# Kernel optimization log

Measured on AMD Instinct MI355X. Metric: run time of the kernel, lower is better.

Reference implementation:

```python
import jax, jax.numpy as jnp
import numpy as np

N_USERS = 100000
N_ITEMS = 50000
N = N_USERS + N_ITEMS  # graph nodes
E = 2_400_000
B = 16384
EMB = 64
HID = 128
LN_EPS = 1e-5


def _gcn(x, W, b, src, dst):
    # PyG GCNConv (eval): sym-normalized aggregation with self-loops.
    xw = x @ W                                      # [N, out]
    deg = jnp.ones((N,), x.dtype).at[dst].add(1.0)  # in-degree + self-loop
    dinv = jax.lax.rsqrt(deg)
    norm = dinv[src] * dinv[dst]                    # [E]
    msg = xw[src] * norm[:, None]                   # [E, out] gather
    out = jax.ops.segment_sum(msg, dst, num_segments=N)
    out = out + xw * (dinv * dinv)[:, None]         # self-loop term (norm_ii = 1/deg_i)
    return out + b


def _ln(h, g, b):
    mu = jnp.mean(h, axis=-1, keepdims=True)
    var = jnp.mean(jnp.square(h - mu), axis=-1, keepdims=True)
    return (h - mu) * jax.lax.rsqrt(var + LN_EPS) * g + b


def setup_inputs() -> dict:
    key = jax.random.key(0)
    ks = jax.random.split(key, 20)
    f32 = jnp.float32
    def lin(k, fi, fo):
        return jax.random.normal(k, (fi, fo), f32) * (1.0 / np.sqrt(fi))
    inp = {
        "x": jax.random.normal(ks[0], (N, EMB), f32),
        "src": jax.random.randint(ks[1], (E,), 0, N, jnp.int32),
        "dst": jax.random.randint(ks[2], (E,), 0, N, jnp.int32),
        "user_indices": jax.random.randint(ks[3], (B,), 1, N_USERS + 1, jnp.int32),
        "item_indices": jax.random.randint(ks[4], (B,), 1, N_ITEMS + 1, jnp.int32),
        # GCNConv weights
        "W1": lin(ks[5], EMB, HID), "b1": jnp.zeros((HID,), f32),
        "W2": lin(ks[6], HID, EMB), "b2": jnp.zeros((EMB,), f32),
        # MLP head: Linear(128,128)-LN-ReLU-Linear(128,64)-LN-ReLU-Linear(64,1)
        "fcW1": lin(ks[7], 2 * EMB, HID), "fcb1": jnp.zeros((HID,), f32),
        "g1": jnp.ones((HID,), f32), "be1": jnp.zeros((HID,), f32),
        "fcW2": lin(ks[8], HID, HID // 2), "fcb2": jnp.zeros((HID // 2,), f32),
        "g2": jnp.ones((HID // 2,), f32), "be2": jnp.zeros((HID // 2,), f32),
        "fcW3": lin(ks[9], HID // 2, 1), "fcb3": jnp.zeros((1,), f32),
    }
    return inp


def reference(x, src, dst, user_indices, item_indices,
              W1, b1, W2, b2,
              fcW1, fcb1, g1, be1, fcW2, fcb2, g2, be2, fcW3, fcb3):
    # graph path (edge_index and x provided); dropout inactive in eval mode
    h = jax.nn.relu(_gcn(x, W1, b1, src, dst))
    h = _gcn(h, W2, b2, src, dst)                   # [N, EMB]
    user_emb = h[:N_USERS][user_indices - 1]        # [B, EMB]
    item_emb = h[N_USERS:][item_indices - 1]        # [B, EMB]
    c = jnp.concatenate([user_emb, item_emb], axis=1)  # [B, 2*EMB]
    z = jax.nn.relu(_ln(c @ fcW1 + fcb1, g1, be1))
    z = jax.nn.relu(_ln(z @ fcW2 + fcb2, g2, be2))
    z = z @ fcW3 + fcb3                             # [B, 1]
    return jax.nn.sigmoid(z).squeeze()
```

## Files before the change

kernel.cpp:

```cpp
#include <hip/hip_runtime.h>
#include <hip/hip_bf16.h>
#include <math.h>

#define N_USERS_C 100000
#define BK_SHIFT 9
#define BK_NODES 512
#define CPAD 16

typedef __bf16 bf8_t __attribute__((ext_vector_type(8)));
typedef float f32x4 __attribute__((ext_vector_type(4)));

__device__ __forceinline__ unsigned int pack_bf16(float a, float b) {
    __hip_bfloat16 ha = __float2bfloat16(a), hb = __float2bfloat16(b);
    return ((unsigned int)(*(unsigned short*)&hb) << 16) | (unsigned int)(*(unsigned short*)&ha);
}
__device__ __forceinline__ unsigned short bf16_1(float a) {
    __hip_bfloat16 ha = __float2bfloat16(a);
    return *(unsigned short*)&ha;
}
__device__ __forceinline__ float bf_lo(unsigned int u) { return __uint_as_float(u << 16); }
__device__ __forceinline__ float bf_hi(unsigned int u) { return __uint_as_float(u & 0xffff0000u); }

__global__ __launch_bounds__(512) void k_pre(const int* __restrict__ dst, int* __restrict__ chist,
                                             const float* __restrict__ x, unsigned int* __restrict__ xb,
                                             const float* __restrict__ W1, const float* __restrict__ W2,
                                             unsigned int* __restrict__ w1p, unsigned int* __restrict__ w2p,
                                             int E, int nbk, int EB2, int n2, int XB) {
    __shared__ int lcnt[BK_NODES];
    const int bid = blockIdx.x;
    const int t = threadIdx.x;
    if (bid < EB2) {
        if (t < nbk) lcnt[t] = 0;
        __syncthreads();
        int e0 = bid * 4096;
        #pragma unroll
        for (int j = 0; j < 8; ++j) {
            int e = e0 + j * 512 + t;
            if (e < E) atomicAdd(&lcnt[dst[e] >> BK_SHIFT], 1);
        }
        __syncthreads();
        if (t < nbk && lcnt[t]) atomicAdd(&chist[t * CPAD], lcnt[t]);
    } else if (bid < EB2 + XB) {
        int base = (bid - EB2) * 2048;
        #pragma unroll
        for (int j = 0; j < 4; ++j) {
            int i = base + j * 512 + t;
            if (i < n2) {
                float2 v = ((const float2*)x)[i];
                xb[i] = pack_bf16(v.x, v.y);
            }
        }
    } else if (bid == EB2 + XB) {
        #pragma unroll
        for (int j = 0; j < 8; ++j) {
            int i = j * 512 + t;
            int kp = i >> 7, n = i & 127;
            w1p[n * 32 + kp] = pack_bf16(W1[(size_t)(2 * kp) * 128 + n],
                                         W1[(size_t)(2 * kp + 1) * 128 + n]);
        }
    } else {
        #pragma unroll
        for (int j = 0; j < 8; ++j) {
            int i = j * 512 + t;
            int kp = i >> 6, n = i & 63;
            w2p[n * 64 + kp] = pack_bf16(W2[(size_t)(2 * kp) * 64 + n],
                                         W2[(size_t)(2 * kp + 1) * 64 + n]);
        }
    }
}

__global__ __launch_bounds__(512) void k_bin(const int* __restrict__ src,
                                             const int* __restrict__ dst,
                                             const int* __restrict__ chist,
                                             int* __restrict__ bcursor0,
                                             int* __restrict__ pairBuf, int E, int nbk) {
    __shared__ int lcnt[BK_NODES];
    __shared__ int lofs[BK_NODES];
    __shared__ int delta[BK_NODES];
    __shared__ int waveSum[8];
    __shared__ int sPack[4096];
    __shared__ unsigned short sBkt[4096];
    const int t = threadIdx.x;
    const int lane = t & 63;
    const int w = t >> 6;
    const int e0 = blockIdx.x * 4096;
    if (t < nbk) lcnt[t] = 0;
    __syncthreads();

    int mySrc[8], myB[8], myDl[8];
    #pragma unroll
    for (int j = 0; j < 8; ++j) {
        int e = e0 + j * 512 + t;
        if (e < E) {
            int sv = src[e], dv = dst[e];
            mySrc[j] = sv; myB[j] = dv >> BK_SHIFT; myDl[j] = dv & (BK_NODES - 1);
            atomicAdd(&lcnt[myB[j]], 1);
        } else myB[j] = -1;
    }
    __syncthreads();

    int v = (t < nbk) ? lcnt[t] : 0;
    int inc = v;
    #pragma unroll
    for (int off = 1; off < 64; off <<= 1) {
        int n = __shfl_up(inc, off);
        if (lane >= off) inc += n;
    }
    if (lane == 63) waveSum[w] = inc;
    int cv = (t < nbk) ? chist[t * CPAD] : 0;
    int cinc = cv;
    #pragma unroll
    for (int off = 1; off < 64; off <<= 1) {
        int n = __shfl_up(cinc, off);
        if (lane >= off) cinc += n;
    }
    __shared__ int cWaveSum[8];
    if (lane == 63) cWaveSum[w] = cinc;
    __syncthreads();
    int wp = 0, cwp = 0;
    #pragma unroll
    for (int i = 0; i < 8; ++i) {
        wp += (i < w) ? waveSum[i] : 0;
        cwp += (i < w) ? cWaveSum[i] : 0;
    }
    int ex = wp + inc - v;
    int cbase = cwp + cinc - cv;
    if (t < nbk) {
        lofs[t] = ex;
        int gb = cbase + ((v > 0) ? atomicAdd(&bcursor0[t * CPAD], v) : 0);
        delta[t] = gb - ex;
    }
    __syncthreads();

    #pragma unroll
    for (int j = 0; j < 8; ++j) {
        if (myB[j] >= 0) {
            int p = atomicAdd(&lofs[myB[j]], 1);
            sPack[p] = mySrc[j] | (myDl[j] << 18);
            sBkt[p] = (unsigned short)myB[j];
        }
    }
    __syncthreads();
    int total = (E - e0 < 4096) ? (E - e0) : 4096;
    for (int i = t; i < total; i += 512)
        pairBuf[delta[sBkt[i]] + i] = sPack[i];
}

__global__ __launch_bounds__(512) void k_bscatter(const int* __restrict__ pairBuf,
                                                  const int* __restrict__ chist,
                                                  int* __restrict__ rowstart,
                                                  float* __restrict__ dinv,
                                                  int* __restrict__ csr,
                                                  unsigned int* __restrict__ xb,
                                                  int N, int E, int nbk) {
    const int b = blockIdx.x;
    const int n0 = b << BK_SHIFT;
    int nn = N - n0; if (nn > BK_NODES) nn = BK_NODES;
    __shared__ int hist[BK_NODES];
    __shared__ int curs[BK_NODES];
    __shared__ float sdv[BK_NODES];
    __shared__ int waveSum[8];
    __shared__ int sE0, sE1;
    const int t = threadIdx.x;
    const int lane = t & 63;
    const int w = t >> 6;

    {
        int cv = (t < nbk) ? chist[t * CPAD] : 0;
        int cinc = cv;
        #pragma unroll
        for (int off = 1; off < 64; off <<= 1) {
            int n = __shfl_up(cinc, off);
            if (lane >= off) cinc += n;
        }
        if (lane == 63) waveSum[w] = cinc;
        if (t < nn) hist[t] = 0;
        __syncthreads();
        int cwp = 0;
        #pragma unroll
        for (int i = 0; i < 8; ++i) cwp += (i < w) ? waveSum[i] : 0;
        if (t == b) { sE0 = cwp + cinc - cv; sE1 = cwp + cinc; }
    }
    __syncthreads();
    const int e0 = sE0, e1 = sE1;

    for (int e = e0 + t; e < e1; e += 512)
        atomicAdd(&hist[pairBuf[e] >> 18], 1);
    __syncthreads();

    int v = (t < nn) ? hist[t] : 0;
    int inc = v;
    #pragma unroll
    for (int off = 1; off < 64; off <<= 1) {
        int n = __shfl_up(inc, off);
        if (lane >= off) inc += n;
    }
    if (lane == 63) waveSum[w] = inc;
    __syncthreads();
    int wp = 0;
    #pragma unroll
    for (int i = 0; i < 8; ++i) wp += (i < w) ? waveSum[i] : 0;
    int ex = wp + inc - v;
    if (t < nn) {
        int r = e0 + ex;
        rowstart[n0 + t] = r;
        curs[t] = r;
        float dv = rsqrtf((float)(v + 1));
        dinv[n0 + t] = dv;
        sdv[t] = dv;
    }
    if (b == gridDim.x - 1 && t == 0) rowstart[N] = E;
    __syncthreads();
    for (int e = e0 + t; e < e1; e += 512) {
        int pk = pairBuf[e];
        int pos = atomicAdd(&curs[pk >> 18], 1);
        csr[pos] = pk & 0x3FFFF;
    }
    {
        uint4* xb4 = (uint4*)(xb + (size_t)n0 * 32);
        int tot = nn * 8;
        for (int j = t; j < tot; j += 512) {
            float dv = sdv[j >> 3];
            uint4 u = xb4[j];
            u.x = pack_bf16(dv * bf_lo(u.x), dv * bf_hi(u.x));
            u.y = pack_bf16(dv * bf_lo(u.y), dv * bf_hi(u.y));
            u.z = pack_bf16(dv * bf_lo(u.z), dv * bf_hi(u.z));
            u.w = pack_bf16(dv * bf_lo(u.w), dv * bf_hi(u.w));
            xb4[j] = u;
        }
    }
}

__global__ __launch_bounds__(256) void k_gather1(const int* __restrict__ rowstart,
                                                 const int* __restrict__ csr,
                                                 const float* __restrict__ dinv,
                                                 const uint4* __restrict__ xb4,
                                                 unsigned int* __restrict__ outb, int N) {
    const int node = blockIdx.x * 4 + (threadIdx.x >> 6);
    const int l = threadIdx.x & 63;
    if (node >= N) return;
    const int sub = l >> 3;
    const int c = l & 7;
    const int rs = rowstart[node];
    const int re = rowstart[node + 1];
    uint4 us = xb4[(size_t)node * 8 + c];
    float dd = dinv[node];

    float acc[8] = {0.f, 0.f, 0.f, 0.f, 0.f, 0.f, 0.f, 0.f};
    for (int base = rs; base < re; base += 64) {
        int idx = base + l;
        int sE = (idx < re) ? csr[idx] : 0;
        int cnt = re - base; if (cnt > 64) cnt = 64;
        int groups = (cnt + 7) >> 3;
        int sk = __shfl(sE, sub);
        uint4 u = xb4[(size_t)sk * 8 + c];
        for (int g = 0; g < groups; ++g) {
            uint4 ucur = u;
            if (g + 1 < groups) {
                int skn = __shfl(sE, (g + 1) * 8 + sub);
                u = xb4[(size_t)skn * 8 + c];
            }
            if (g * 8 + sub < cnt) {
                acc[0] += bf_lo(ucur.x); acc[1] += bf_hi(ucur.x);
                acc[2] += bf_lo(ucur.y); acc[3] += bf_hi(ucur.y);
                acc[4] += bf_lo(ucur.z); acc[5] += bf_hi(ucur.z);
                acc[6] += bf_lo(ucur.w); acc[7] += bf_hi(ucur.w);
            }
        }
    }
    #pragma unroll
    for (int m = 8; m < 64; m <<= 1)
        #pragma unroll
        for (int i = 0; i < 8; ++i) acc[i] += __shfl_xor(acc[i], m);
    if (sub == 0) {
        uint4 o;
        o.x = pack_bf16(dd * (acc[0] + bf_lo(us.x)), dd * (acc[1] + bf_hi(us.x)));
        o.y = pack_bf16(dd * (acc[2] + bf_lo(us.y)), dd * (acc[3] + bf_hi(us.y)));
        o.z = pack_bf16(dd * (acc[4] + bf_lo(us.z)), dd * (acc[5] + bf_hi(us.z)));
        o.w = pack_bf16(dd * (acc[6] + bf_lo(us.w)), dd * (acc[7] + bf_hi(us.w)));
        ((uint4*)outb)[(size_t)node * 8 + c] = o;
    }
}

__global__ __launch_bounds__(256) void k_layer12(const unsigned int* __restrict__ aggXb,
                                                 const unsigned int* __restrict__ w1p,
                                                 const float* __restrict__ b1,
                                                 const unsigned int* __restrict__ w2p,
                                                 const float* __restrict__ dinv,
                                                 unsigned int* __restrict__ xs2b, int N) {
    __shared__ unsigned int sA[64 * 36];
    __shared__ unsigned int sB[128 * 36];
    __shared__ unsigned int sC[64 * 68];
    const int t = threadIdx.x;
    const int w = t >> 6;
    const int l = t & 63;
    const int n16 = l & 15;
    const int quad = l >> 4;
    const int row0 = blockIdx.x * 64;

    for (int i = t; i < 512; i += 256) {
        int r = i >> 3, c = i & 7;
        int row = row0 + r;
        uint4 u = (row < N) ? ((const uint4*)aggXb)[(size_t)row * 8 + c]
                            : make_uint4(0u, 0u, 0u, 0u);
        *(uint4*)&sA[r * 36 + c * 4] = u;
    }
    {
        const uint4* w1p4 = (const uint4*)w1p;
        for (int j = t; j < 1024; j += 256) {
            int n = j >> 3, kp4 = j & 7;
            *(uint4*)&sB[n * 36 + kp4 * 4] = w1p4[j];
        }
    }
    __syncthreads();

    f32x4 acc[8];
    #pragma unroll
    for (int nt = 0; nt < 8; ++nt) acc[nt] = (f32x4){0.f, 0.f, 0.f, 0.f};
    {
        const int am = w * 16 + n16;
        bf8_t a0 = *(const bf8_t*)&sA[am * 36 + quad * 4];
        bf8_t a1 = *(const bf8_t*)&sA[am * 36 + 16 + quad * 4];
        #pragma unroll
        for (int nt = 0; nt < 8; ++nt) {
            bf8_t b0 = *(const bf8_t*)&sB[(nt * 16 + n16) * 36 + quad * 4];
            bf8_t b1v = *(const bf8_t*)&sB[(nt * 16 + n16) * 36 + 16 + quad * 4];
            acc[nt] = __builtin_amdgcn_mfma_f32_16x16x32_bf16(a0, b0, acc[nt], 0, 0, 0);
            acc[nt] = __builtin_amdgcn_mfma_f32_16x16x32_bf16(a1, b1v, acc[nt], 0, 0, 0);
        }
    }
    __syncthreads();

    {
        unsigned short* sC16 = (unsigned short*)sC;
        #pragma unroll
        for (int nt = 0; nt < 8; ++nt) {
            int col = nt * 16 + n16;
            float bv = b1[col];
            #pragma unroll
            for (int reg = 0; reg < 4; ++reg) {
                int r = w * 16 + quad * 4 + reg;
                sC16[r * 136 + col] = bf16_1(fmaxf(acc[nt][reg] + bv, 0.f));
            }
        }
    }
    {
        const uint4* w2p4 = (const uint4*)w2p;
        for (int j = t; j < 1024; j += 256) {
            int n = j >> 4, kp4 = j & 15;
            *(uint4*)&sB[n * 68 + kp4 * 4] = w2p4[j];
        }
    }
    __syncthreads();

    f32x4 acc2[4];
    #pragma unroll
    for (int nt = 0; nt < 4; ++nt) acc2[nt] = (f32x4){0.f, 0.f, 0.f, 0.f};
    {
        const int am = w * 16 + n16;
        #pragma unroll
        for (int ks = 0; ks < 4; ++ks) {
            bf8_t a = *(const bf8_t*)&sC[am * 68 + ks * 16 + quad * 4];
            #pragma unroll
            for (int nt = 0; nt < 4; ++nt) {
                bf8_t b = *(const bf8_t*)&sB[(nt * 16 + n16) * 68 + ks * 16 + quad * 4];
                acc2[nt] = __builtin_amdgcn_mfma_f32_16x16x32_bf16(a, b, acc2[nt], 0, 0, 0);
            }
        }
    }

    __syncthreads();
    {
        unsigned short* sA16 = (unsigned short*)sA;
        #pragma unroll
        for (int reg = 0; reg < 4; ++reg) {
            int r = w * 16 + quad * 4 + reg;
            int row = row0 + r;
            float dd = (row < N) ? dinv[row] : 0.f;
            #pragma unroll
            for (int nt = 0; nt < 4; ++nt)
                sA16[r * 72 + nt * 16 + n16] = bf16_1(acc2[nt][reg] * dd);
        }
    }
    __syncthreads();
    for (int i = t; i < 512; i += 256) {
        int r = i >> 3, c = i & 7;
        int row = row0 + r;
        if (row < N)
            ((uint4*)xs2b)[(size_t)row * 8 + c] = *(uint4*)&sA[r * 36 + c * 4];
    }
}

__global__ __launch_bounds__(256) void k_gather_pairs(const int* __restrict__ rowstart,
                                                      const int* __restrict__ csr,
                                                      const float* __restrict__ dinv,
                                                      const uint4* __restrict__ xs2b4,
                                                      const float* __restrict__ b2,
                                                      const int* __restrict__ ui,
                                                      const int* __restrict__ ii,
                                                      float* __restrict__ cB, int B) {
    const int wave = threadIdx.x >> 6;
    const int b = blockIdx.x * 2 + (wave >> 1);
    const int half = wave & 1;
    const int l = threadIdx.x & 63;
    const int sub = l >> 3;
    const int c = l & 7;
    if (b >= B) return;
    const int node = (half == 0) ? (ui[b] - 1) : (N_USERS_C + ii[b] - 1);
    const int rs = rowstart[node];
    const int re = rowstart[node + 1];
    uint4 us = xs2b4[(size_t)node * 8 + c];
    float dd = dinv[node];

    float acc[8] = {0.f, 0.f, 0.f, 0.f, 0.f, 0.f, 0.f, 0.f};
    for (int base = rs; base < re; base += 64) {
        int idx = base + l;
        int sE = (idx < re) ? csr[idx] : 0;
        int cnt = re - base; if (cnt > 64) cnt = 64;
        int groups = (cnt + 7) >> 3;
        int sk = __shfl(sE, sub);
        uint4 u = xs2b4[(size_t)sk * 8 + c];
        for (int g = 0; g < groups; ++g) {
            uint4 ucur = u;
            if (g + 1 < groups) {
                int skn = __shfl(sE, (g + 1) * 8 + sub);
                u = xs2b4[(size_t)skn * 8 + c];
            }
            if (g * 8 + sub < cnt) {
                acc[0] += bf_lo(ucur.x); acc[1] += bf_hi(ucur.x);
                acc[2] += bf_lo(ucur.y); acc[3] += bf_hi(ucur.y);
                acc[4] += bf_lo(ucur.z); acc[5] += bf_hi(ucur.z);
                acc[6] += bf_lo(ucur.w); acc[7] += bf_hi(ucur.w);
            }
        }
    }
    #pragma unroll
    for (int m = 8; m < 64; m <<= 1)
        #pragma unroll
        for (int i = 0; i < 8; ++i) acc[i] += __shfl_xor(acc[i], m);
    if (sub == 0) {
        float4 s0, s1;
        s0.x = bf_lo(us.x); s0.y = bf_hi(us.x); s0.z = bf_lo(us.y); s0.w = bf_hi(us.y);
        s1.x = bf_lo(us.z); s1.y = bf_hi(us.z); s1.z = bf_lo(us.w); s1.w = bf_hi(us.w);
        float4 bb0 = ((const float4*)b2)[c * 2];
        float4 bb1 = ((const float4*)b2)[c * 2 + 1];
        float4 o0, o1;
        o0.x = dd * (acc[0] + s0.x) + bb0.x;
        o0.y = dd * (acc[1] + s0.y) + bb0.y;
        o0.z = dd * (acc[2] + s0.z) + bb0.z;
        o0.w = dd * (acc[3] + s0.w) + bb0.w;
        o1.x = dd * (acc[4] + s1.x) + bb1.x;
        o1.y = dd * (acc[5] + s1.y) + bb1.y;
        o1.z = dd * (acc[6] + s1.z) + bb1.z;
        o1.w = dd * (acc[7] + s1.w) + bb1.w;
        ((float4*)cB)[(size_t)b * 32 + half * 16 + c * 2] = o0;
        ((float4*)cB)[(size_t)b * 32 + half * 16 + c * 2 + 1] = o1;
    }
}

__global__ __launch_bounds__(256) void k_mlp(const float* __restrict__ cB,
                                             const float* __restrict__ fcW1, const float* __restrict__ fcb1,
                                             const float* __restrict__ g1,   const float* __restrict__ be1,
                                             const float* __restrict__ fcW2, const float* __restrict__ fcb2,
                                             const float* __restrict__ g2,   const float* __restrict__ be2,
                                             const float* __restrict__ fcW3, const float* __restrict__ fcb3,
                                             float* __restrict__ out) {
    __shared__ float sIn[32 * 128];
    __shared__ float sW[64 * 128];
    const int t = threadIdx.x;
    const int row0 = blockIdx.x * 32;
    const int rg = t >> 4;
    const int cg = t & 15;

    for (int i = t; i < 1024; i += 256) {
        int r = i >> 5, c4 = i & 31;
        *(float4*)&sIn[r * 128 + c4 * 4] = *(const float4*)&cB[(size_t)(row0 + r) * 128 + c4 * 4];
    }

    float acc1[2][8];
    {
        float4 b01 = *(const float4*)&fcb1[cg * 8];
        float4 b23 = *(const float4*)&fcb1[cg * 8 + 4];
        #pragma unroll
        for (int jj = 0; jj < 2; ++jj) {
            acc1[jj][0] = b01.x; acc1[jj][1] = b01.y; acc1[jj][2] = b01.z; acc1[jj][3] = b01.w;
            acc1[jj][4] = b23.x; acc1[jj][5] = b23.y; acc1[jj][6] = b23.z; acc1[jj][7] = b23.w;
        }
    }
    for (int s = 0; s < 2; ++s) {
        __syncthreads();
        for (int i = t; i < 2048; i += 256) {
            int k = i >> 5, c4 = i & 31;
            *(float4*)&sW[k * 128 + c4 * 4] = *(const float4*)&fcW1[(size_t)(64 * s + k) * 128 + c4 * 4];
        }
        __syncthreads();
        for (int k0 = 0; k0 < 64; k0 += 4) {
            float4 a[2];
            #pragma unroll
            for (int jj = 0; jj < 2; ++jj)
                a[jj] = *(const float4*)&sIn[(rg * 2 + jj) * 128 + 64 * s + k0];
            #pragma unroll
            for (int kk = 0; kk < 4; ++kk) {
                float4 w0 = *(const float4*)&sW[(k0 + kk) * 128 + cg * 8];
                float4 w1 = *(const float4*)&sW[(k0 + kk) * 128 + cg * 8 + 4];
                #pragma unroll
                for (int jj = 0; jj < 2; ++jj) {
                    float f = ((const float*)&a[jj])[kk];
                    acc1[jj][0] += f * w0.x; acc1[jj][1] += f * w0.y;
                    acc1[jj][2] += f * w0.z; acc1[jj][3] += f * w0.w;
                    acc1[jj][4] += f * w1.x; acc1[jj][5] += f * w1.y;
                    acc1[jj][6] += f * w1.z; acc1[jj][7] += f * w1.w;
                }
            }
        }
    }
    __syncthreads();

    {
        float4 g01 = *(const float4*)&g1[cg * 8];
        float4 g23 = *(const float4*)&g1[cg * 8 + 4];
        float4 e01 = *(const float4*)&be1[cg * 8];
        float4 e23 = *(const float4*)&be1[cg * 8 + 4];
        float gv[8] = {g01.x, g01.y, g01.z, g01.w, g23.x, g23.y, g23.z, g23.w};
        float ev[8] = {e01.x, e01.y, e01.z, e01.w, e23.x, e23.y, e23.z, e23.w};
        #pragma unroll
        for (int jj = 0; jj < 2; ++jj) {
            float s_ = 0.f, ss = 0.f;
            #pragma unroll
            for (int c = 0; c < 8; ++c) { float v = acc1[jj][c]; s_ += v; ss += v * v; }
            #pragma unroll
            for (int m = 1; m < 16; m <<= 1) { s_ += __shfl_xor(s_, m); ss += __shfl_xor(ss, m); }
            float mu = s_ * (1.0f / 128.0f);
            float var = ss * (1.0f / 128.0f) - mu * mu;
            float rs = rsqrtf(var + 1e-5f);
            #pragma unroll
            for (int c = 0; c < 8; ++c) {
                float z = (acc1[jj][c] - mu) * rs * gv[c] + ev[c];
                sIn[(rg * 2 + jj) * 128 + cg * 8 + c] = fmaxf(z, 0.f);
            }
        }
    }
    __syncthreads();

    for (int i = t; i < 2048; i += 256) {
        int k = i >> 4, c4 = i & 15;
        *(float4*)&sW[k * 64 + c4 * 4] = *(const float4*)&fcW2[(size_t)k * 64 + c4 * 4];
    }
    float acc2[2][4];
    {
        float4 bv = *(const float4*)&fcb2[cg * 4];
        #pragma unroll
        for (int jj = 0; jj < 2; ++jj) {
            acc2[jj][0] = bv.x; acc2[jj][1] = bv.y; acc2[jj][2] = bv.z; acc2[jj][3] = bv.w;
        }
    }
    __syncthreads();
    for (int k0 = 0; k0 < 128; k0 += 4) {
        float4 a[2], w[4];
        #pragma unroll
        for (int jj = 0; jj < 2; ++jj) a[jj] = *(const float4*)&sIn[(rg * 2 + jj) * 128 + k0];
        #pragma unroll
        for (int kk = 0; kk < 4; ++kk) w[kk] = *(const float4*)&sW[(k0 + kk) * 64 + cg * 4];
        #pragma unroll
        for (int jj = 0; jj < 2; ++jj) {
            const float* aj = (const float*)&a[jj];
            #pragma unroll
            for (int kk = 0; kk < 4; ++kk) {
                float f = aj[kk];
                acc2[jj][0] += f * w[kk].x; acc2[jj][1] += f * w[kk].y;
                acc2[jj][2] += f * w[kk].z; acc2[jj][3] += f * w[kk].w;
            }
        }
    }

    {
        float4 gv4 = *(const float4*)&g2[cg * 4];
        float4 ev4 = *(const float4*)&be2[cg * 4];
        float4 w34 = *(const float4*)&fcW3[cg * 4];
        float gv[4] = {gv4.x, gv4.y, gv4.z, gv4.w};
        float ev[4] = {ev4.x, ev4.y, ev4.z, ev4.w};
        float wv[4] = {w34.x, w34.y, w34.z, w34.w};
        float b3 = fcb3[0];
        #pragma unroll
        for (int jj = 0; jj < 2; ++jj) {
            float s_ = 0.f, ss = 0.f;
            #pragma unroll
            for (int c = 0; c < 4; ++c) { float v = acc2[jj][c]; s_ += v; ss += v * v; }
            #pragma unroll
            for (int m = 1; m < 16; m <<= 1) { s_ += __shfl_xor(s_, m); ss += __shfl_xor(ss, m); }
            float mu = s_ * (1.0f / 64.0f);
            float var = ss * (1.0f / 64.0f) - mu * mu;
            float rs = rsqrtf(var + 1e-5f);
            float p = 0.f;
            #pragma unroll
            for (int c = 0; c < 4; ++c) {
                float z = fmaxf((acc2[jj][c] - mu) * rs * gv[c] + ev[c], 0.f);
                p += z * wv[c];
            }
            #pragma unroll
            for (int m = 1; m < 16; m <<= 1) p += __shfl_xor(p, m);
            if (cg == 0) out[row0 + rg * 2 + jj] = 1.0f / (1.0f + expf(-(p + b3)));
        }
    }
}

extern "C" void kernel_launch(void* const* d_in, const int* in_sizes, int n_in,
                              void* d_out, int out_size, void* d_ws, size_t ws_size,
                              hipStream_t stream) {
    const float* x    = (const float*)d_in[0];
    const int*   src  = (const int*)d_in[1];
    const int*   dst  = (const int*)d_in[2];
    const int*   ui   = (const int*)d_in[3];
    const int*   ii   = (const int*)d_in[4];
    const float* W1   = (const float*)d_in[5];
    const float* b1   = (const float*)d_in[6];
    const float* W2   = (const float*)d_in[7];
    const float* b2   = (const float*)d_in[8];
    const float* fcW1 = (const float*)d_in[9];
    const float* fcb1 = (const float*)d_in[10];
    const float* g1   = (const float*)d_in[11];
    const float* be1  = (const float*)d_in[12];
    const float* fcW2 = (const float*)d_in[13];
    const float* fcb2 = (const float*)d_in[14];
    const float* g2   = (const float*)d_in[15];
    const float* be2  = (const float*)d_in[16];
    const float* fcW3 = (const float*)d_in[17];
    const float* fcb3 = (const float*)d_in[18];
    float* out = (float*)d_out;

    const int N = in_sizes[0] / 64;
    const int E = in_sizes[1];
    const int B = in_sizes[3];
    const int NBK = (N + BK_NODES - 1) >> BK_SHIFT;
    const int EB2 = (E + 4095) / 4096;
    const int n2 = N * 32;
    const int XB = (n2 + 2047) / 2048;

    float* ws   = (float*)d_ws;
    float* dinv = ws;
    int* rowstart = (int*)(dinv + N);
    int* csr      = rowstart + (N + 1);
    unsigned int* xb = (unsigned int*)(csr + E);
    unsigned int* bufU = xb + (size_t)N * 32;
    unsigned int* xs2b = bufU + (size_t)N * 32;
    float* cB = (float*)(xs2b + (size_t)N * 32);
    unsigned int* w1p = (unsigned int*)(cB + (size_t)B * 128);
    unsigned int* w2p = w1p + 4096;
    int* pairBuf = (int*)bufU;
    int* chist   = pairBuf + E;
    int* bcursor = chist + 512 * CPAD;
    unsigned int* aggXb = bufU;

    hipMemsetAsync(chist, 0, 2 * 512 * CPAD * sizeof(int), stream);
    k_pre<<<EB2 + XB + 2, 512, 0, stream>>>(dst, chist, x, xb, W1, W2, w1p, w2p,
                                            E, NBK, EB2, n2, XB);
    k_bin<<<EB2, 512, 0, stream>>>(src, dst, chist, bcursor, pairBuf, E, NBK);
    k_bscatter<<<NBK, 512, 0, stream>>>(pairBuf, chist, rowstart, dinv, csr, xb, N, E, NBK);

    k_gather1<<<(N + 3) / 4, 256, 0, stream>>>(rowstart, csr, dinv, (const uint4*)xb, aggXb, N);

    k_layer12<<<(N + 63) / 64, 256, 0, stream>>>(aggXb, w1p, b1, w2p, dinv, xs2b, N);

    k_gather_pairs<<<(B + 1) / 2, 256, 0, stream>>>(rowstart, csr, dinv, (const uint4*)xs2b,
                                                    b2, ui, ii, cB, B);

    k_mlp<<<B / 32, 256, 0, stream>>>(cB, fcW1, fcb1, g1, be1,
                                      fcW2, fcb2, g2, be2, fcW3, fcb3, out);
}
```

Measured before the change: 335.8 us.

## Split waves into half-wave node workers and unroll bucket scatter loops

The two neighbor-gather kernels now assign one node per 32-lane half-wave instead of one per 64-lane wave, with 4 edges in flight per step instead of 8. Average degree is about 16, so full-wave processing left many lanes idle. The bucket scatter kernel also unrolls its histogram, CSR scatter and row-scaling loops by four and two to put more loads in flight. Exposed latency per node is higher for high-degree nodes, and the shuffle indexing now depends on the half-wave offset.

New measurement: 332.3 us. About the same (-1.0%).

```diff
diff --git a/kernel.cpp b/kernel.cpp
--- a/kernel.cpp
+++ b/kernel.cpp
@@ -184,8 +184,19 @@
     __syncthreads();
     const int e0 = sE0, e1 = sE1;
 
-    for (int e = e0 + t; e < e1; e += 512)
-        atomicAdd(&hist[pairBuf[e] >> 18], 1);
+    {
+        int e = e0 + t;
+        for (; e + 1536 < e1; e += 2048) {
+            int p0 = pairBuf[e], p1 = pairBuf[e + 512];
+            int p2 = pairBuf[e + 1024], p3 = pairBuf[e + 1536];
+            atomicAdd(&hist[p0 >> 18], 1);
+            atomicAdd(&hist[p1 >> 18], 1);
+            atomicAdd(&hist[p2 >> 18], 1);
+            atomicAdd(&hist[p3 >> 18], 1);
+        }
+        for (; e < e1; e += 512)
+            atomicAdd(&hist[pairBuf[e] >> 18], 1);
+    }
     __syncthreads();
 
     int v = (t < nn) ? hist[t] : 0;
@@ -211,22 +222,45 @@
     }
     if (b == gridDim.x - 1 && t == 0) rowstart[N] = E;
     __syncthreads();
-    for (int e = e0 + t; e < e1; e += 512) {
-        int pk = pairBuf[e];
-        int pos = atomicAdd(&curs[pk >> 18], 1);
-        csr[pos] = pk & 0x3FFFF;
+    {
+        int e = e0 + t;
+        for (; e + 1536 < e1; e += 2048) {
+            int p0 = pairBuf[e], p1 = pairBuf[e + 512];
+            int p2 = pairBuf[e + 1024], p3 = pairBuf[e + 1536];
+            int q0 = atomicAdd(&curs[p0 >> 18], 1); csr[q0] = p0 & 0x3FFFF;
+            int q1 = atomicAdd(&curs[p1 >> 18], 1); csr[q1] = p1 & 0x3FFFF;
+            int q2 = atomicAdd(&curs[p2 >> 18], 1); csr[q2] = p2 & 0x3FFFF;
+            int q3 = atomicAdd(&curs[p3 >> 18], 1); csr[q3] = p3 & 0x3FFFF;
+        }
+        for (; e < e1; e += 512) {
+            int pk = pairBuf[e];
+            int pos = atomicAdd(&curs[pk >> 18], 1);
+            csr[pos] = pk & 0x3FFFF;
+        }
     }
     {
         uint4* xb4 = (uint4*)(xb + (size_t)n0 * 32);
         int tot = nn * 8;
-        for (int j = t; j < tot; j += 512) {
+        for (int j = t; j < tot; j += 1024) {
+            int j2 = j + 512;
+            uint4 u = xb4[j];
+            uint4 u2;
+            bool two = (j2 < tot);
+            if (two) u2 = xb4[j2];
             float dv = sdv[j >> 3];
-            uint4 u = xb4[j];
             u.x = pack_bf16(dv * bf_lo(u.x), dv * bf_hi(u.x));
             u.y = pack_bf16(dv * bf_lo(u.y), dv * bf_hi(u.y));
             u.z = pack_bf16(dv * bf_lo(u.z), dv * bf_hi(u.z));
             u.w = pack_bf16(dv * bf_lo(u.w), dv * bf_hi(u.w));
             xb4[j] = u;
+            if (two) {
+                float dv2 = sdv[j2 >> 3];
+                u2.x = pack_bf16(dv2 * bf_lo(u2.x), dv2 * bf_hi(u2.x));
+                u2.y = pack_bf16(dv2 * bf_lo(u2.y), dv2 * bf_hi(u2.y));
+                u2.z = pack_bf16(dv2 * bf_lo(u2.z), dv2 * bf_hi(u2.z));
+                u2.w = pack_bf16(dv2 * bf_lo(u2.w), dv2 * bf_hi(u2.w));
+                xb4[j2] = u2;
+            }
         }
     }
 }
@@ -236,31 +270,34 @@
                                                  const float* __restrict__ dinv,
                                                  const uint4* __restrict__ xb4,
                                                  unsigned int* __restrict__ outb, int N) {
-    const int node = blockIdx.x * 4 + (threadIdx.x >> 6);
     const int l = threadIdx.x & 63;
+    const int w = threadIdx.x >> 6;
+    const int half = l >> 5;
+    const int h = l & 31;
+    const int sub = h >> 3;
+    const int c = h & 7;
+    const int node = blockIdx.x * 8 + w * 2 + half;
     if (node >= N) return;
-    const int sub = l >> 3;
-    const int c = l & 7;
     const int rs = rowstart[node];
     const int re = rowstart[node + 1];
     uint4 us = xb4[(size_t)node * 8 + c];
     float dd = dinv[node];
 
     float acc[8] = {0.f, 0.f, 0.f, 0.f, 0.f, 0.f, 0.f, 0.f};
-    for (int base = rs; base < re; base += 64) {
-        int idx = base + l;
+    for (int base = rs; base < re; base += 32) {
+        int idx = base + h;
         int sE = (idx < re) ? csr[idx] : 0;
-        int cnt = re - base; if (cnt > 64) cnt = 64;
-        int groups = (cnt + 7) >> 3;
-        int sk = __shfl(sE, sub);
+        int cnt = re - base; if (cnt > 32) cnt = 32;
+        int groups = (cnt + 3) >> 2;
+        int sk = __shfl(sE, half * 32 + sub);
         uint4 u = xb4[(size_t)sk * 8 + c];
         for (int g = 0; g < groups; ++g) {
             uint4 ucur = u;
             if (g + 1 < groups) {
-                int skn = __shfl(sE, (g + 1) * 8 + sub);
+                int skn = __shfl(sE, half * 32 + (g + 1) * 4 + sub);
                 u = xb4[(size_t)skn * 8 + c];
             }
-            if (g * 8 + sub < cnt) {
+            if (g * 4 + sub < cnt) {
                 acc[0] += bf_lo(ucur.x); acc[1] += bf_hi(ucur.x);
                 acc[2] += bf_lo(ucur.y); acc[3] += bf_hi(ucur.y);
                 acc[4] += bf_lo(ucur.z); acc[5] += bf_hi(ucur.z);
@@ -269,7 +306,7 @@
         }
     }
     #pragma unroll
-    for (int m = 8; m < 64; m <<= 1)
+    for (int m = 8; m < 32; m <<= 1)
         #pragma unroll
         for (int i = 0; i < 8; ++i) acc[i] += __shfl_xor(acc[i], m);
     if (sub == 0) {
@@ -399,12 +436,13 @@
                                                       const int* __restrict__ ui,
                                                       const int* __restrict__ ii,
                                                       float* __restrict__ cB, int B) {
-    const int wave = threadIdx.x >> 6;
-    const int b = blockIdx.x * 2 + (wave >> 1);
-    const int half = wave & 1;
+    const int w = threadIdx.x >> 6;
+    const int b = blockIdx.x * 4 + w;
     const int l = threadIdx.x & 63;
-    const int sub = l >> 3;
-    const int c = l & 7;
+    const int half = l >> 5;
+    const int h = l & 31;
+    const int sub = h >> 3;
+    const int c = h & 7;
     if (b >= B) return;
     const int node = (half == 0) ? (ui[b] - 1) : (N_USERS_C + ii[b] - 1);
     const int rs = rowstart[node];
@@ -413,20 +451,20 @@
     float dd = dinv[node];
 
     float acc[8] = {0.f, 0.f, 0.f, 0.f, 0.f, 0.f, 0.f, 0.f};
-    for (int base = rs; base < re; base += 64) {
-        int idx = base + l;
+    for (int base = rs; base < re; base += 32) {
+        int idx = base + h;
         int sE = (idx < re) ? csr[idx] : 0;
-        int cnt = re - base; if (cnt > 64) cnt = 64;
-        int groups = (cnt + 7) >> 3;
-        int sk = __shfl(sE, sub);
+        int cnt = re - base; if (cnt > 32) cnt = 32;
+        int groups = (cnt + 3) >> 2;
+        int sk = __shfl(sE, half * 32 + sub);
         uint4 u = xs2b4[(size_t)sk * 8 + c];
         for (int g = 0; g < groups; ++g) {
             uint4 ucur = u;
             if (g + 1 < groups) {
-                int skn = __shfl(sE, (g + 1) * 8 + sub);
+                int skn = __shfl(sE, half * 32 + (g + 1) * 4 + sub);
                 u = xs2b4[(size_t)skn * 8 + c];
             }
-            if (g * 8 + sub < cnt) {
+            if (g * 4 + sub < cnt) {
                 acc[0] += bf_lo(ucur.x); acc[1] += bf_hi(ucur.x);
                 acc[2] += bf_lo(ucur.y); acc[3] += bf_hi(ucur.y);
                 acc[4] += bf_lo(ucur.z); acc[5] += bf_hi(ucur.z);
@@ -435,7 +473,7 @@
         }
     }
     #pragma unroll
-    for (int m = 8; m < 64; m <<= 1)
+    for (int m = 8; m < 32; m <<= 1)
         #pragma unroll
         for (int i = 0; i < 8; ++i) acc[i] += __shfl_xor(acc[i], m);
     if (sub == 0) {
@@ -657,11 +695,11 @@
     k_bin<<<EB2, 512, 0, stream>>>(src, dst, chist, bcursor, pairBuf, E, NBK);
     k_bscatter<<<NBK, 512, 0, stream>>>(pairBuf, chist, rowstart, dinv, csr, xb, N, E, NBK);
 
-    k_gather1<<<(N + 3) / 4, 256, 0, stream>>>(rowstart, csr, dinv, (const uint4*)xb, aggXb, N);
+    k_gather1<<<(N + 7) / 8, 256, 0, stream>>>(rowstart, csr, dinv, (const uint4*)xb, aggXb, N);
 
     k_layer12<<<(N + 63) / 64, 256, 0, stream>>>(aggXb, w1p, b1, w2p, dinv, xs2b, N);
 
-    k_gather_pairs<<<(B + 1) / 2, 256, 0, stream>>>(rowstart, csr, dinv, (const uint4*)xs2b,
+    k_gather_pairs<<<(B + 3) / 4, 256, 0, stream>>>(rowstart, csr, dinv, (const uint4*)xs2b,
                                                     b2, ui, ii, cB, B);
 
     k_mlp<<<B / 32, 256, 0, stream>>>(cB, fcW1, fcb1, g1, be1,
```
